# Performance work log

Measured on AMD Instinct MI355X. Metric: run time of the kernel, lower is better.

Reference implementation:

```python
import jax, jax.numpy as jnp
import numpy as np

B, S, IN, EMB, H = 4, 2048, 256, 512, 8
D = EMB // H
SCALE = 1.0 / np.sqrt(EMB)  # source uses 1/sqrt(embed_size), not head_dim
EPS = 1e-5


def setup_inputs() -> dict:
    key = jax.random.key(0)
    ks = jax.random.split(key, 20)
    def w(k, shape, fan_in):
        return jax.random.normal(k, shape, jnp.float32) * (1.0 / np.sqrt(fan_in))
    inp = {"state_emb": jax.random.normal(ks[0], (B, S, IN), jnp.float32)}
    i = 1
    for p in ("q", "k", "v"):
        inp[f"{p}_W1"] = w(ks[i], (IN, EMB), IN); i += 1
        inp[f"{p}_b1"] = jnp.zeros((EMB,), jnp.float32)
        inp[f"{p}_W2"] = w(ks[i], (EMB, EMB), EMB); i += 1
        inp[f"{p}_b2"] = jnp.zeros((EMB,), jnp.float32)
    inp["f_W1"] = w(ks[i], (EMB, 2 * EMB), EMB); i += 1
    inp["f_b1"] = jnp.zeros((2 * EMB,), jnp.float32)
    inp["f_W2"] = w(ks[i], (2 * EMB, EMB), 2 * EMB); i += 1
    inp["f_b2"] = jnp.zeros((EMB,), jnp.float32)
    inp["ln1_g"] = jnp.ones((EMB,), jnp.float32)
    inp["ln1_b"] = jnp.zeros((EMB,), jnp.float32)
    inp["ln2_g"] = jnp.ones((EMB,), jnp.float32)
    inp["ln2_b"] = jnp.zeros((EMB,), jnp.float32)
    return inp


def _mlp2(x, W1, b1, W2, b2):
    return jax.nn.relu(x @ W1 + b1) @ W2 + b2


def _layernorm(x, g, b):
    mu = jnp.mean(x, axis=-1, keepdims=True)
    var = jnp.mean(jnp.square(x - mu), axis=-1, keepdims=True)
    return (x - mu) * jax.lax.rsqrt(var + EPS) * g + b


def reference(state_emb, q_W1, q_b1, q_W2, q_b2, k_W1, k_b1, k_W2, k_b2,
              v_W1, v_b1, v_W2, v_b2, f_W1, f_b1, f_W2, f_b2,
              ln1_g, ln1_b, ln2_g, ln2_b):
    n, dim = state_emb.shape[0], state_emb.shape[1]
    q = _mlp2(state_emb, q_W1, q_b1, q_W2, q_b2)  # [n, dim, EMB]
    k = _mlp2(state_emb, k_W1, k_b1, k_W2, k_b2)
    v = _mlp2(state_emb, v_W1, v_b1, v_W2, v_b2)
    qh = q.reshape(n, dim, H, D)
    kh = k.reshape(n, dim, H, D)
    vh = v.reshape(n, dim, H, D)
    energy = jnp.einsum('nqhd,nkhd->nhqk', qh, kh)  # [n, H, dim, dim]
    attn = jax.nn.softmax(energy * SCALE, axis=-1)
    ctx = jnp.einsum('nhql,nlhd->nqhd', attn, vh).reshape(n, dim, EMB)
    x = _layernorm(ctx + q, ln1_g, ln1_b)  # residual with queries, per source
    ff = _mlp2(x, f_W1, f_b1, f_W2, f_b2)
    return _layernorm(x + ff, ln2_g, ln2_b)
```

## Files before the change

### kernel.cpp

```cpp
#include <hip/hip_runtime.h>
#include <hip/hip_bf16.h>
#include <math.h>

#define BB   4
#define SS   2048
#define INF_ 256
#define EMB  512
#define NH   8
#define HD   64
#define NT   8192

typedef unsigned short u16;
typedef unsigned int   u32;
typedef __attribute__((ext_vector_type(8))) short bf16x8;
typedef __attribute__((ext_vector_type(8))) unsigned short u16x8;
typedef __attribute__((ext_vector_type(4))) float f32x4;

constexpr float C2  = 0.06375871607f;
constexpr float RB  = 0.005624549f;
constexpr float TB  = 1.00390625f;
constexpr float EPS = 1e-5f;

__device__ __forceinline__ u16 f2bf(float v) {
    __hip_bfloat16 h = __float2bfloat16(v);
    return *(u16*)&h;
}
__device__ __forceinline__ float bf2f(u16 u) {
    __hip_bfloat16 h = *(__hip_bfloat16*)&u;
    return __bfloat162float(h);
}
__device__ __forceinline__ u16 ftrunc_bf(float v) {
    return (u16)(__float_as_uint(v * TB) >> 16);
}
__device__ __forceinline__ f32x4 mfma16(bf16x8 a, bf16x8 b, f32x4 c) {
    return __builtin_amdgcn_mfma_f32_16x16x32_bf16(a, b, c, 0, 0, 0);
}
__device__ __forceinline__ void async16(const void* g, void* l) {
    __builtin_amdgcn_global_load_lds(
        (const __attribute__((address_space(1))) void*)g,
        (__attribute__((address_space(3))) void*)l, 16, 0, 0);
}
__device__ __forceinline__ int derive_flag(const u16* x) {
    const int lane = threadIdx.x & 63;
    const unsigned e = (x[lane * 2] >> 7) & 0xFF;
    float pl = (e == 0 || (e >= 110 && e <= 140)) ? 1.0f : 0.0f;
    #pragma unroll
    for (int o = 1; o < 64; o <<= 1) pl += __shfl_xor(pl, o);
    return pl < 32.0f;
}

__global__ __launch_bounds__(256) void prep(
    const u16* __restrict__ xsrc,
    const void* w0, const void* w1, const void* w2, const void* w3,
    const void* w4, const void* w5, const void* w6, const void* w7,
    const void* p0, const void* p1, const void* p2, const void* p3,
    const void* p4, const void* p5, const void* p6, const void* p7,
    const void* p8, const void* p9, const void* p10, const void* p11,
    u16* __restrict__ xbf, u16* __restrict__ wt1, u16* __restrict__ wt2,
    u16* __restrict__ f1t, u16* __restrict__ f2t, float* __restrict__ small)
{
    const int isf = derive_flag(xsrc);
    const int z = blockIdx.z;
    const int tid = threadIdx.x;

    if (z < 8) {
        int K, M; const void* src; u16* dst;
        switch (z) {
            case 0: K=256;  M=512;  src=w0; dst=wt1;             break;
            case 1: K=256;  M=512;  src=w1; dst=wt1+512*256;     break;
            case 2: K=256;  M=512;  src=w2; dst=wt1+2*512*256;   break;
            case 3: K=512;  M=512;  src=w3; dst=wt2;             break;
            case 4: K=512;  M=512;  src=w4; dst=wt2+512*512;     break;
            case 5: K=512;  M=512;  src=w5; dst=wt2+2*512*512;   break;
            case 6: K=512;  M=1024; src=w6; dst=f1t;             break;
            default:K=1024; M=512;  src=w7; dst=f2t;             break;
        }
        const int m0 = blockIdx.x * 32, k0 = blockIdx.y * 32;
        if (m0 >= M || k0 >= K) return;
        __shared__ u16 t[32][33];
        const int tx = tid & 31, ty = tid >> 5;
        #pragma unroll
        for (int i = 0; i < 4; ++i) {
            const int kk = k0 + ty + i * 8;
            t[ty + i * 8][tx] = isf ? ftrunc_bf(((const float*)src)[(size_t)kk * M + m0 + tx])
                                    : ((const u16*)src)[(size_t)kk * M + m0 + tx];
        }
        __syncthreads();
        #pragma unroll
        for (int i = 0; i < 4; ++i) {
            const int mm = m0 + ty + i * 8;
            dst[(size_t)mm * K + k0 + tx] = t[tx][ty + i * 8];
        }
    } else if (z == 8) {
        const int bid = blockIdx.y * 32 + blockIdx.x;
        const int base = bid * 2048 + tid * 8;
        if (isf) {
            #pragma unroll
            for (int j = 0; j < 8; ++j)
                xbf[base + j] = ftrunc_bf(((const float*)xsrc)[base + j]);
        } else {
            *(u16x8*)&xbf[base] = *(const u16x8*)&xsrc[base];
        }
    } else {
        const int bid = blockIdx.y * 32 + blockIdx.x;
        if (bid >= 28) return;
        const int e = bid * 256 + tid;
        int id, i;
        if (e < 3072)      { id = e >> 9;               i = e & 511;          }
        else if (e < 4096) { id = 6;                    i = e - 3072;         }
        else               { id = 7 + ((e - 4096) >> 9); i = (e - 4096) & 511; }
        const void* src;
        switch (id) {
            case 0: src = p0; break;  case 1: src = p1; break;
            case 2: src = p2; break;  case 3: src = p3; break;
            case 4: src = p4; break;  case 5: src = p5; break;
            case 6: src = p6; break;  case 7: src = p7; break;
            case 8: src = p8; break;  case 9: src = p9; break;
            case 10: src = p10; break; default: src = p11; break;
        }
        small[e] = isf ? ((const float*)src)[i] : bf2f(((const u16*)src)[i]);
    }
}

__global__ __launch_bounds__(256) void transpose_v(
    const u16* __restrict__ v, u16* __restrict__ vt)
{
    __shared__ u16 t[32][33];
    const int tid = threadIdx.x, tx = tid & 31, ty = tid >> 5;
    const int s0 = blockIdx.x * 32, d0 = blockIdx.y * 32;
    const int bh = blockIdx.z, b = bh >> 3, h = bh & 7;
    #pragma unroll
    for (int i = 0; i < 4; ++i) {
        const int s = s0 + ty + i * 8;
        t[ty + i * 8][tx] = v[((size_t)b * SS + s) * EMB + h * HD + d0 + tx];
    }
    __syncthreads();
    #pragma unroll
    for (int i = 0; i < 4; ++i) {
        const int d = d0 + ty + i * 8;
        vt[((size_t)bh * HD + d) * SS + s0 + tx] = t[tx][ty + i * 8];
    }
}

template <int TR, int TC, bool RELU, bool AWHICH>
__global__ __launch_bounds__(256) void gemm_bt(
    const u16* __restrict__ Aall, const u16* __restrict__ Wtall,
    const float* __restrict__ ball, u16* __restrict__ out,
    int N, int K, int M)
{
    constexpr int RT = TR / 32, CT = TC / 32;
    constexpr int AR = TR / 32, BR = TC / 32;
    __shared__ __align__(16) u16 sA[TR * 64];
    __shared__ __align__(16) u16 sB[TC * 64];

    const int mtiles = M / TC;
    const int which = blockIdx.x / mtiles;
    const int colb  = blockIdx.x % mtiles;
    const int row0 = blockIdx.y * TR, col0 = colb * TC;
    const u16* A  = Aall + (AWHICH ? (size_t)which * N * K : 0);
    const u16* Wt = Wtall + (size_t)which * M * K;
    const float* bias = ball + (size_t)which * M;

    const int tid = threadIdx.x;
    const int lane = tid & 63, w = tid >> 6;
    const int wrow = (w & 1) * (TR / 2), wcol = (w >> 1) * (TC / 2);
    const int c = lane & 15, quad = lane >> 4;

    const u16* ap[AR]; const u16* bp[BR];
    #pragma unroll
    for (int i = 0; i < AR; ++i) {
        const int raw = i * 256 + tid, r = raw >> 3, ch = (raw & 7) ^ (r & 7);
        ap[i] = A + (size_t)(row0 + r) * K + ch * 8;
    }
    #pragma unroll
    for (int i = 0; i < BR; ++i) {
        const int raw = i * 256 + tid, r = raw >> 3, ch = (raw & 7) ^ (r & 7);
        bp[i] = Wt + (size_t)(col0 + r) * K + ch * 8;
    }

    f32x4 acc[RT][CT] = {};

    for (int k0 = 0; k0 < K; k0 += 64) {
        __syncthreads();
        #pragma unroll
        for (int i = 0; i < AR; ++i) {
            async16(ap[i], (char*)sA + (i * 256 + tid) * 16);
            ap[i] += 64;
        }
        #pragma unroll
        for (int i = 0; i < BR; ++i) {
            async16(bp[i], (char*)sB + (i * 256 + tid) * 16);
            bp[i] += 64;
        }
        __syncthreads();

        #pragma unroll
        for (int kt = 0; kt < 2; ++kt) {
            bf16x8 af[RT], bfr[CT];
            #pragma unroll
            for (int rt = 0; rt < RT; ++rt) {
                const int r = wrow + rt * 16 + c;
                af[rt] = *(const bf16x8*)&sA[(r * 8 + ((kt * 4 + quad) ^ (r & 7))) * 8];
            }
            #pragma unroll
            for (int ct = 0; ct < CT; ++ct) {
                const int r = wcol + ct * 16 + c;
                bfr[ct] = *(const bf16x8*)&sB[(r * 8 + ((kt * 4 + quad) ^ (r & 7))) * 8];
            }
            #pragma unroll
            for (int rt = 0; rt < RT; ++rt)
                #pragma unroll
                for (int ct = 0; ct < CT; ++ct)
                    acc[rt][ct] = mfma16(af[rt], bfr[ct], acc[rt][ct]);
        }
    }

    const size_t outW = (size_t)which * N * M;
    #pragma unroll
    for (int rt = 0; rt < RT; ++rt) {
        #pragma unroll
        for (int i = 0; i < 4; ++i) {
            const int row = row0 + wrow + rt * 16 + quad * 4 + i;
            #pragma unroll
            for (int ct = 0; ct < CT; ++ct) {
                const int col = col0 + wcol + ct * 16 + c;
                float v = acc[rt][ct][i] + bias[col];
                if (RELU) v = fmaxf(v, 0.0f);
                out[outW + (size_t)row * M + col] = (u16)(__float_as_uint(v * TB) >> 16);
            }
        }
    }
}

__global__ __launch_bounds__(256) void attn_mfma(
    const u16* __restrict__ q, const u16* __restrict__ k,
    const u16* __restrict__ vt, u16* __restrict__ ctx)
{
    __shared__ __align__(16) u16 sK[64 * 64];
    __shared__ __align__(16) u16 sV[64 * 64];
    __shared__ __align__(16) u16 sP[4][16 * 64];

    const int tid = threadIdx.x;
    const int w = tid >> 6, lane = tid & 63;
    const int c = lane & 15, quad = lane >> 4;
    const int q0 = blockIdx.x * 64;
    const int h = blockIdx.y, b = blockIdx.z;
    const size_t tokbase = (size_t)b * SS;
    const int hoff = h * HD;

    const int myq = q0 + w * 16 + c;
    bf16x8 qf[2];
    #pragma unroll
    for (int kt = 0; kt < 2; ++kt)
        qf[kt] = *(const bf16x8*)&q[(tokbase + myq) * EMB + hoff + kt * 32 + quad * 8];

    const u16* kp[2]; const u16* vp[2];
    #pragma unroll
    for (int i = 0; i < 2; ++i) {
        const int raw = i * 256 + tid, rr = raw >> 3, ch = (raw & 7) ^ (rr & 7);
        kp[i] = k + (tokbase + rr) * EMB + hoff + ch * 8;
        vp[i] = vt + ((size_t)(b * NH + h) * HD + rr) * SS + ch * 8;
    }

    float l_lane = 0.0f;
    f32x4 accO[4] = {};

    for (int t = 0; t < SS / 64; ++t) {
        __syncthreads();
        #pragma unroll
        for (int i = 0; i < 2; ++i) {
            async16(kp[i], (char*)sK + (i * 256 + tid) * 16);
            kp[i] += 64 * EMB;
        }
        #pragma unroll
        for (int i = 0; i < 2; ++i) {
            async16(vp[i], (char*)sV + (i * 256 + tid) * 16);
            vp[i] += 64;
        }
        __syncthreads();

        f32x4 accS[4] = {};
        #pragma unroll
        for (int mt = 0; mt < 4; ++mt) {
            const int key = mt * 16 + c;
            #pragma unroll
            for (int kt = 0; kt < 2; ++kt) {
                bf16x8 kf = *(const bf16x8*)&sK[(key * 8 + ((kt * 4 + quad) ^ (key & 7))) * 8];
                accS[mt] = mfma16(kf, qf[kt], accS[mt]);
            }
        }

        u32 pw[8];
        float ls = 0.0f;
        #pragma unroll
        for (int mt = 0; mt < 4; ++mt) {
            const float e0 = __builtin_amdgcn_exp2f(fmaf(accS[mt][0], C2, RB));
            const float e1 = __builtin_amdgcn_exp2f(fmaf(accS[mt][1], C2, RB));
            const float e2 = __builtin_amdgcn_exp2f(fmaf(accS[mt][2], C2, RB));
            const float e3 = __builtin_amdgcn_exp2f(fmaf(accS[mt][3], C2, RB));
            ls += (e0 + e1) + (e2 + e3);
            pw[2 * mt]     = __builtin_amdgcn_perm(__float_as_uint(e1), __float_as_uint(e0), 0x07060302u);
            pw[2 * mt + 1] = __builtin_amdgcn_perm(__float_as_uint(e3), __float_as_uint(e2), 0x07060302u);
        }
        l_lane += ls;

        #pragma unroll
        for (int mt = 0; mt < 4; ++mt) {
            const int chunkW = (quad >> 1) + 2 * mt;
            const int blk = c * 8 + (chunkW ^ (c & 7));
            uint2 u; u.x = pw[2 * mt]; u.y = pw[2 * mt + 1];
            *(uint2*)((char*)&sP[w][0] + blk * 16 + 8 * (quad & 1)) = u;
        }

        bf16x8 pf[2];
        #pragma unroll
        for (int kt = 0; kt < 2; ++kt)
            pf[kt] = *(const bf16x8*)&sP[w][(c * 8 + ((kt * 4 + quad) ^ (c & 7))) * 8];
        #pragma unroll
        for (int nt = 0; nt < 4; ++nt) {
            const int d = nt * 16 + c;
            #pragma unroll
            for (int kt = 0; kt < 2; ++kt) {
                bf16x8 vf = *(const bf16x8*)&sV[(d * 8 + ((kt * 4 + quad) ^ (d & 7))) * 8];
                accO[nt] = mfma16(pf[kt], vf, accO[nt]);
            }
        }
    }

    float l = l_lane;
    l += __shfl_xor(l, 16);
    l += __shfl_xor(l, 32);
    float li[4];
    #pragma unroll
    for (int i = 0; i < 4; ++i) {
        const float lv = __shfl(l, quad * 4 + i, 16);
        li[i] = (lv > 0.0f) ? (1.0f / lv) : 0.0f;
    }
    #pragma unroll
    for (int nt = 0; nt < 4; ++nt)
        #pragma unroll
        for (int i = 0; i < 4; ++i) {
            const int tok = q0 + w * 16 + quad * 4 + i;
            ctx[(tokbase + tok) * EMB + hoff + nt * 16 + c] =
                (u16)(__float_as_uint(accO[nt][i] * li[i] * TB) >> 16);
        }
}

__global__ __launch_bounds__(256) void ln_mid(
    const u16* __restrict__ a, const u16* __restrict__ b2,
    const float* __restrict__ g, const float* __restrict__ be,
    u16* __restrict__ outb)
{
    const int wave = threadIdx.x >> 6, lane = threadIdx.x & 63;
    const size_t row = (size_t)blockIdx.x * 4 + wave;
    const u16x8 av = *(const u16x8*)&a[row * EMB + lane * 8];
    const u16x8 bv = *(const u16x8*)&b2[row * EMB + lane * 8];
    float vals[8], sum = 0.0f;
    #pragma unroll
    for (int i = 0; i < 8; ++i) { vals[i] = bf2f(av[i]) + bf2f(bv[i]); sum += vals[i]; }
    #pragma unroll
    for (int o = 1; o < 64; o <<= 1) sum += __shfl_xor(sum, o);
    const float mu = sum * (1.0f / 512.0f);
    float vs = 0.0f;
    #pragma unroll
    for (int i = 0; i < 8; ++i) { const float d = vals[i] - mu; vs += d * d; }
    #pragma unroll
    for (int o = 1; o < 64; o <<= 1) vs += __shfl_xor(vs, o);
    const float rstd = rsqrtf(vs * (1.0f / 512.0f) + EPS);
    u16x8 ov;
    #pragma unroll
    for (int i = 0; i < 8; ++i) {
        const int col = lane * 8 + i;
        ov[i] = f2bf((vals[i] - mu) * rstd * g[col] + be[col]);
    }
    *(u16x8*)&outb[row * EMB + lane * 8] = ov;
}

__global__ __launch_bounds__(256) void ln_final(
    const u16* __restrict__ a, const u16* __restrict__ b2,
    const float* __restrict__ g, const float* __restrict__ be,
    void* __restrict__ dout, const u16* __restrict__ xsrc)
{
    const int isf = derive_flag(xsrc);
    const int wave = threadIdx.x >> 6, lane = threadIdx.x & 63;
    const size_t row = (size_t)blockIdx.x * 4 + wave;
    const u16x8 av = *(const u16x8*)&a[row * EMB + lane * 8];
    const u16x8 bv = *(const u16x8*)&b2[row * EMB + lane * 8];
    float vals[8], sum = 0.0f;
    #pragma unroll
    for (int i = 0; i < 8; ++i) { vals[i] = bf2f(av[i]) + bf2f(bv[i]); sum += vals[i]; }
    #pragma unroll
    for (int o = 1; o < 64; o <<= 1) sum += __shfl_xor(sum, o);
    const float mu = sum * (1.0f / 512.0f);
    float vs = 0.0f;
    #pragma unroll
    for (int i = 0; i < 8; ++i) { const float d = vals[i] - mu; vs += d * d; }
    #pragma unroll
    for (int o = 1; o < 64; o <<= 1) vs += __shfl_xor(vs, o);
    const float rstd = rsqrtf(vs * (1.0f / 512.0f) + EPS);
    if (isf) {
        #pragma unroll
        for (int i = 0; i < 8; ++i) {
            const int col = lane * 8 + i;
            ((float*)dout)[row * EMB + col] = (vals[i] - mu) * rstd * g[col] + be[col];
        }
    } else {
        u16x8 ov;
        #pragma unroll
        for (int i = 0; i < 8; ++i) {
            const int col = lane * 8 + i;
            ov[i] = f2bf((vals[i] - mu) * rstd * g[col] + be[col]);
        }
        *(u16x8*)&((u16*)dout)[row * EMB + lane * 8] = ov;
    }
}

extern "C" void kernel_launch(void* const* d_in, const int* in_sizes, int n_in,
                              void* d_out, int out_size, void* d_ws, size_t ws_size,
                              hipStream_t stream)
{
    char* ws = (char*)d_ws;
    float* small = (float*)(ws + 0);
    u16*   wt1   = (u16*)(ws + 32768);
    u16*   wt2   = (u16*)(ws + 819200);
    u16*   f1t   = (u16*)(ws + 2392064);
    u16*   f2t   = (u16*)(ws + 3440640);
    u16*   xbf   = (u16*)(ws + 4489216);
    u16*   h3    = (u16*)(ws + 8683520);
    u16*   qkv   = (u16*)(ws + 33849344);
    u16*   vtb   = (u16*)(ws + 59015168);
    u16*   ctxb  = (u16*)(ws + 67403776);
    u16*   x1b   = (u16*)(ws + 75792384);
    u16*   ffb   = (u16*)(ws + 84180992);

    const dim3 blk(256);
    const u16* xsrc = (const u16*)d_in[0];

    prep<<<dim3(32, 32, 10), blk, 0, stream>>>(
        xsrc,
        d_in[1], d_in[5], d_in[9], d_in[3], d_in[7], d_in[11], d_in[13], d_in[15],
        d_in[2], d_in[6], d_in[10], d_in[4], d_in[8], d_in[12],
        d_in[14], d_in[16], d_in[17], d_in[18], d_in[19], d_in[20],
        xbf, wt1, wt2, f1t, f2t, small);

    gemm_bt<128, 128, true, false><<<dim3(12, 64), blk, 0, stream>>>(
        xbf, wt1, small + 0, h3, NT, INF_, EMB);
    gemm_bt<128, 128, false, true><<<dim3(12, 64), blk, 0, stream>>>(
        h3, wt2, small + 1536, qkv, NT, EMB, EMB);

    transpose_v<<<dim3(64, 2, 32), blk, 0, stream>>>(qkv + 2 * (size_t)NT * EMB, vtb);

    attn_mfma<<<dim3(SS / 64, NH, BB), blk, 0, stream>>>(
        qkv, qkv + (size_t)NT * EMB, vtb, ctxb);

    ln_mid<<<NT / 4, blk, 0, stream>>>(ctxb, qkv, small + 4608, small + 5120, x1b);

    u16* h2 = h3;
    gemm_bt<128, 128, true, false><<<dim3(8, 64), blk, 0, stream>>>(
        x1b, f1t, small + 3072, h2, NT, EMB, 1024);
    gemm_bt<128, 64, false, false><<<dim3(8, 64), blk, 0, stream>>>(
        h2, f2t, small + 4096, ffb, NT, 1024, EMB);

    ln_final<<<NT / 4, blk, 0, stream>>>(x1b, ffb, small + 5632, small + 6144, d_out, xsrc);
}
```

Measured before the change: 263.1 us.

## Fuse V transpose into QKV GEMM epilogue and double-buffer attention tiles

```diff
diff --git a/kernel.cpp b/kernel.cpp
--- a/kernel.cpp
+++ b/kernel.cpp
@@ -122,36 +122,19 @@
     }
 }
 
-__global__ __launch_bounds__(256) void transpose_v(
-    const u16* __restrict__ v, u16* __restrict__ vt)
-{
-    __shared__ u16 t[32][33];
-    const int tid = threadIdx.x, tx = tid & 31, ty = tid >> 5;
-    const int s0 = blockIdx.x * 32, d0 = blockIdx.y * 32;
-    const int bh = blockIdx.z, b = bh >> 3, h = bh & 7;
-    #pragma unroll
-    for (int i = 0; i < 4; ++i) {
-        const int s = s0 + ty + i * 8;
-        t[ty + i * 8][tx] = v[((size_t)b * SS + s) * EMB + h * HD + d0 + tx];
-    }
-    __syncthreads();
-    #pragma unroll
-    for (int i = 0; i < 4; ++i) {
-        const int d = d0 + ty + i * 8;
-        vt[((size_t)bh * HD + d) * SS + s0 + tx] = t[tx][ty + i * 8];
-    }
-}
-
-template <int TR, int TC, bool RELU, bool AWHICH>
+template <int TR, int TC, bool RELU, bool AWHICH, bool VOUT>
 __global__ __launch_bounds__(256) void gemm_bt(
     const u16* __restrict__ Aall, const u16* __restrict__ Wtall,
     const float* __restrict__ ball, u16* __restrict__ out,
-    int N, int K, int M)
+    u16* __restrict__ vtb, int N, int K, int M)
 {
     constexpr int RT = TR / 32, CT = TC / 32;
     constexpr int AR = TR / 32, BR = TC / 32;
-    __shared__ __align__(16) u16 sA[TR * 64];
-    __shared__ __align__(16) u16 sB[TC * 64];
+    constexpr int SSTAGE = (TR + TC) * 64;
+    constexpr int SELEMS = VOUT ? (SSTAGE > 128 * 136 ? SSTAGE : 128 * 136) : SSTAGE;
+    __shared__ __align__(16) u16 smem[SELEMS];
+    u16* sA = smem;
+    u16* sB = smem + TR * 64;
 
     const int mtiles = M / TC;
     const int which = blockIdx.x / mtiles;
@@ -215,6 +198,33 @@
         }
     }
 
+    if (VOUT && which == 2) {
+        __syncthreads();
+        #pragma unroll
+        for (int rt = 0; rt < RT; ++rt) {
+            const int rowb = wrow + rt * 16 + quad * 4;
+            #pragma unroll
+            for (int ct = 0; ct < CT; ++ct) {
+                const int col = wcol + ct * 16 + c;
+                ushort4 pk;
+                pk.x = ftrunc_bf(acc[rt][ct][0] + bias[col0 + col]);
+                pk.y = ftrunc_bf(acc[rt][ct][1] + bias[col0 + col]);
+                pk.z = ftrunc_bf(acc[rt][ct][2] + bias[col0 + col]);
+                pk.w = ftrunc_bf(acc[rt][ct][3] + bias[col0 + col]);
+                *(ushort4*)&smem[col * 136 + rowb] = pk;
+            }
+        }
+        __syncthreads();
+        const int dl = tid >> 1, half = tid & 1;
+        const int hg = (col0 + dl) >> 6, dd = (col0 + dl) & 63;
+        const int bb = row0 >> 11, s0 = row0 & 2047;
+        u16* dst = vtb + ((size_t)(bb * NH + hg) * HD + dd) * SS + s0 + half * 64;
+        #pragma unroll
+        for (int j = 0; j < 8; ++j)
+            *(u16x8*)&dst[j * 8] = *(const u16x8*)&smem[dl * 136 + half * 64 + j * 8];
+        return;
+    }
+
     const size_t outW = (size_t)which * N * M;
     #pragma unroll
     for (int rt = 0; rt < RT; ++rt) {
@@ -226,7 +236,7 @@
                 const int col = col0 + wcol + ct * 16 + c;
                 float v = acc[rt][ct][i] + bias[col];
                 if (RELU) v = fmaxf(v, 0.0f);
-                out[outW + (size_t)row * M + col] = (u16)(__float_as_uint(v * TB) >> 16);
+                out[outW + (size_t)row * M + col] = ftrunc_bf(v);
             }
         }
     }
@@ -236,23 +246,29 @@
     const u16* __restrict__ q, const u16* __restrict__ k,
     const u16* __restrict__ vt, u16* __restrict__ ctx)
 {
-    __shared__ __align__(16) u16 sK[64 * 64];
-    __shared__ __align__(16) u16 sV[64 * 64];
-    __shared__ __align__(16) u16 sP[4][16 * 64];
+    __shared__ __align__(16) u16 sK[2][64 * 64];
+    __shared__ __align__(16) u16 sV[2][64 * 64];
+    __shared__ __align__(16) u16 sP[4][32 * 64];
 
     const int tid = threadIdx.x;
     const int w = tid >> 6, lane = tid & 63;
     const int c = lane & 15, quad = lane >> 4;
-    const int q0 = blockIdx.x * 64;
-    const int h = blockIdx.y, b = blockIdx.z;
+    const int id = blockIdx.x;
+    const int slot = id >> 3;
+    const int bh = ((id & 7) << 2) | (slot >> 4);
+    const int qt = slot & 15;
+    const int b = bh >> 3, h = bh & 7;
+    const int q0 = qt * 128;
     const size_t tokbase = (size_t)b * SS;
     const int hoff = h * HD;
 
-    const int myq = q0 + w * 16 + c;
-    bf16x8 qf[2];
-    #pragma unroll
-    for (int kt = 0; kt < 2; ++kt)
-        qf[kt] = *(const bf16x8*)&q[(tokbase + myq) * EMB + hoff + kt * 32 + quad * 8];
+    bf16x8 qf[2][2];
+    #pragma unroll
+    for (int f = 0; f < 2; ++f)
+        #pragma unroll
+        for (int kt = 0; kt < 2; ++kt)
+            qf[f][kt] = *(const bf16x8*)&q[(tokbase + q0 + w * 32 + f * 16 + c) * EMB
+                                           + hoff + kt * 32 + quad * 8];
 
     const u16* kp[2]; const u16* vp[2];
     #pragma unroll
@@ -261,89 +277,102 @@
         kp[i] = k + (tokbase + rr) * EMB + hoff + ch * 8;
         vp[i] = vt + ((size_t)(b * NH + h) * HD + rr) * SS + ch * 8;
     }
-
-    float l_lane = 0.0f;
-    f32x4 accO[4] = {};
+    auto stage = [&](int buf) {
+        #pragma unroll
+        for (int i = 0; i < 2; ++i) {
+            async16(kp[i], (char*)sK[buf] + (i * 256 + tid) * 16);
+            kp[i] += 64 * EMB;
+        }
+        #pragma unroll
+        for (int i = 0; i < 2; ++i) {
+            async16(vp[i], (char*)sV[buf] + (i * 256 + tid) * 16);
+            vp[i] += 64;
+        }
+    };
+    stage(0);
+
+    float l0 = 0.0f, l1 = 0.0f;
+    f32x4 accO[2][4] = {};
 
     for (int t = 0; t < SS / 64; ++t) {
         __syncthreads();
-        #pragma unroll
-        for (int i = 0; i < 2; ++i) {
-            async16(kp[i], (char*)sK + (i * 256 + tid) * 16);
-            kp[i] += 64 * EMB;
-        }
-        #pragma unroll
-        for (int i = 0; i < 2; ++i) {
-            async16(vp[i], (char*)sV + (i * 256 + tid) * 16);
-            vp[i] += 64;
-        }
-        __syncthreads();
-
-        f32x4 accS[4] = {};
+        const int buf = t & 1;
+        if (t < SS / 64 - 1) stage(buf ^ 1);
+
+        f32x4 accS[2][4] = {};
         #pragma unroll
         for (int mt = 0; mt < 4; ++mt) {
             const int key = mt * 16 + c;
             #pragma unroll
             for (int kt = 0; kt < 2; ++kt) {
-                bf16x8 kf = *(const bf16x8*)&sK[(key * 8 + ((kt * 4 + quad) ^ (key & 7))) * 8];
-                accS[mt] = mfma16(kf, qf[kt], accS[mt]);
-            }
-        }
-
-        u32 pw[8];
-        float ls = 0.0f;
-        #pragma unroll
-        for (int mt = 0; mt < 4; ++mt) {
-            const float e0 = __builtin_amdgcn_exp2f(fmaf(accS[mt][0], C2, RB));
-            const float e1 = __builtin_amdgcn_exp2f(fmaf(accS[mt][1], C2, RB));
-            const float e2 = __builtin_amdgcn_exp2f(fmaf(accS[mt][2], C2, RB));
-            const float e3 = __builtin_amdgcn_exp2f(fmaf(accS[mt][3], C2, RB));
-            ls += (e0 + e1) + (e2 + e3);
-            pw[2 * mt]     = __builtin_amdgcn_perm(__float_as_uint(e1), __float_as_uint(e0), 0x07060302u);
-            pw[2 * mt + 1] = __builtin_amdgcn_perm(__float_as_uint(e3), __float_as_uint(e2), 0x07060302u);
-        }
-        l_lane += ls;
-
-        #pragma unroll
-        for (int mt = 0; mt < 4; ++mt) {
-            const int chunkW = (quad >> 1) + 2 * mt;
-            const int blk = c * 8 + (chunkW ^ (c & 7));
-            uint2 u; u.x = pw[2 * mt]; u.y = pw[2 * mt + 1];
-            *(uint2*)((char*)&sP[w][0] + blk * 16 + 8 * (quad & 1)) = u;
-        }
-
-        bf16x8 pf[2];
-        #pragma unroll
-        for (int kt = 0; kt < 2; ++kt)
-            pf[kt] = *(const bf16x8*)&sP[w][(c * 8 + ((kt * 4 + quad) ^ (c & 7))) * 8];
+                bf16x8 kf = *(const bf16x8*)&sK[buf][(key * 8 + ((kt * 4 + quad) ^ (key & 7))) * 8];
+                accS[0][mt] = mfma16(kf, qf[0][kt], accS[0][mt]);
+                accS[1][mt] = mfma16(kf, qf[1][kt], accS[1][mt]);
+            }
+        }
+
+        #pragma unroll
+        for (int f = 0; f < 2; ++f) {
+            const int row = f * 16 + c;
+            float ls = 0.0f;
+            u32 pw[8];
+            #pragma unroll
+            for (int mt = 0; mt < 4; ++mt) {
+                const float e0 = __builtin_amdgcn_exp2f(fmaf(accS[f][mt][0], C2, RB));
+                const float e1 = __builtin_amdgcn_exp2f(fmaf(accS[f][mt][1], C2, RB));
+                const float e2 = __builtin_amdgcn_exp2f(fmaf(accS[f][mt][2], C2, RB));
+                const float e3 = __builtin_amdgcn_exp2f(fmaf(accS[f][mt][3], C2, RB));
+                ls += (e0 + e1) + (e2 + e3);
+                pw[2 * mt]     = __builtin_amdgcn_perm(__float_as_uint(e1), __float_as_uint(e0), 0x07060302u);
+                pw[2 * mt + 1] = __builtin_amdgcn_perm(__float_as_uint(e3), __float_as_uint(e2), 0x07060302u);
+            }
+            if (f == 0) l0 += ls; else l1 += ls;
+            #pragma unroll
+            for (int mt = 0; mt < 4; ++mt) {
+                const int chunk = 2 * mt + (quad >> 1);
+                uint2 u; u.x = pw[2 * mt]; u.y = pw[2 * mt + 1];
+                *(uint2*)((char*)&sP[w][0] + (row * 8 + (chunk ^ (c & 7))) * 16 + 8 * (quad & 1)) = u;
+            }
+        }
+
+        bf16x8 pf[2][2];
+        #pragma unroll
+        for (int f = 0; f < 2; ++f)
+            #pragma unroll
+            for (int kt = 0; kt < 2; ++kt)
+                pf[f][kt] = *(const bf16x8*)&sP[w][((f * 16 + c) * 8 + ((kt * 4 + quad) ^ (c & 7))) * 8];
         #pragma unroll
         for (int nt = 0; nt < 4; ++nt) {
             const int d = nt * 16 + c;
             #pragma unroll
             for (int kt = 0; kt < 2; ++kt) {
-                bf16x8 vf = *(const bf16x8*)&sV[(d * 8 + ((kt * 4 + quad) ^ (d & 7))) * 8];
-                accO[nt] = mfma16(pf[kt], vf, accO[nt]);
-            }
-        }
-    }
-
-    float l = l_lane;
-    l += __shfl_xor(l, 16);
-    l += __shfl_xor(l, 32);
-    float li[4];
-    #pragma unroll
-    for (int i = 0; i < 4; ++i) {
-        const float lv = __shfl(l, quad * 4 + i, 16);
-        li[i] = (lv > 0.0f) ? (1.0f / lv) : 0.0f;
-    }
-    #pragma unroll
-    for (int nt = 0; nt < 4; ++nt)
+                bf16x8 vf = *(const bf16x8*)&sV[buf][(d * 8 + ((kt * 4 + quad) ^ (d & 7))) * 8];
+                accO[0][nt] = mfma16(pf[0][kt], vf, accO[0][nt]);
+                accO[1][nt] = mfma16(pf[1][kt], vf, accO[1][nt]);
+            }
+        }
+    }
+
+    #pragma unroll
+    for (int f = 0; f < 2; ++f) {
+        float l = (f == 0) ? l0 : l1;
+        l += __shfl_xor(l, 16);
+        l += __shfl_xor(l, 32);
+        float li[4];
         #pragma unroll
         for (int i = 0; i < 4; ++i) {
-            const int tok = q0 + w * 16 + quad * 4 + i;
-            ctx[(tokbase + tok) * EMB + hoff + nt * 16 + c] =
-                (u16)(__float_as_uint(accO[nt][i] * li[i] * TB) >> 16);
-        }
+            const float lv = __shfl(l, quad * 4 + i, 16);
+            li[i] = (lv > 0.0f) ? (1.0f / lv) : 0.0f;
+        }
+        #pragma unroll
+        for (int nt = 0; nt < 4; ++nt)
+            #pragma unroll
+            for (int i = 0; i < 4; ++i) {
+                const int tok = q0 + w * 32 + f * 16 + quad * 4 + i;
+                ctx[(tokbase + tok) * EMB + hoff + nt * 16 + c] =
+                    ftrunc_bf(accO[f][nt][i] * li[i]);
+            }
+    }
 }
 
 __global__ __launch_bounds__(256) void ln_mid(
@@ -443,23 +472,21 @@
         d_in[14], d_in[16], d_in[17], d_in[18], d_in[19], d_in[20],
         xbf, wt1, wt2, f1t, f2t, small);
 
-    gemm_bt<128, 128, true, false><<<dim3(12, 64), blk, 0, stream>>>(
-        xbf, wt1, small + 0, h3, NT, INF_, EMB);
-    gemm_bt<128, 128, false, true><<<dim3(12, 64), blk, 0, stream>>>(
-        h3, wt2, small + 1536, qkv, NT, EMB, EMB);
-
-    transpose_v<<<dim3(64, 2, 32), blk, 0, stream>>>(qkv + 2 * (size_t)NT * EMB, vtb);
-
-    attn_mfma<<<dim3(SS / 64, NH, BB), blk, 0, stream>>>(
+    gemm_bt<128, 128, true, false, false><<<dim3(12, 64), blk, 0, stream>>>(
+        xbf, wt1, small + 0, h3, nullptr, NT, INF_, EMB);
+    gemm_bt<128, 128, false, true, true><<<dim3(12, 64), blk, 0, stream>>>(
+        h3, wt2, small + 1536, qkv, vtb, NT, EMB, EMB);
+
+    attn_mfma<<<dim3(512), blk, 0, stream>>>(
         qkv, qkv + (size_t)NT * EMB, vtb, ctxb);
 
     ln_mid<<<NT / 4, blk, 0, stream>>>(ctxb, qkv, small + 4608, small + 5120, x1b);
 
     u16* h2 = h3;
-    gemm_bt<128, 128, true, false><<<dim3(8, 64), blk, 0, stream>>>(
-        x1b, f1t, small + 3072, h2, NT, EMB, 1024);
-    gemm_bt<128, 64, false, false><<<dim3(8, 64), blk, 0, stream>>>(
-        h2, f2t, small + 4096, ffb, NT, 1024, EMB);
+    gemm_bt<128, 128, true, false, false><<<dim3(8, 64), blk, 0, stream>>>(
+        x1b, f1t, small + 3072, h2, nullptr, NT, EMB, 1024);
+    gemm_bt<128, 64, false, false, false><<<dim3(8, 64), blk, 0, stream>>>(
+        h2, f2t, small + 4096, ffb, nullptr, NT, 1024, EMB);
 
     ln_final<<<NT / 4, blk, 0, stream>>>(x1b, ffb, small + 5632, small + 6144, d_out, xsrc);
 }
```

After: 260.6 us. Within noise of the previous version (-1.0%).
